# Kernel optimization log

Measured on AMD Instinct MI355X. Metric: run time of the kernel, lower is better.

Reference implementation:

```python
import jax, jax.numpy as jnp
import numpy as np

DIM = 256
N_STATE = 8
DT_RANK = 16  # ceil(dim/16)
D_CONV = 4
HIDDEN = 128  # dim * rank_ratio
EPS = 1e-6


def rmsnorm(x, w):
    # matches torch: x / (||x||_2 / sqrt(d) + eps) * w
    norm = jnp.sqrt(jnp.sum(x * x, axis=-1, keepdims=True))
    return x / (norm / np.sqrt(x.shape[-1]) + EPS) * w


def dwconv1d(x, w, b, pad_l, pad_r):
    # x: (b, l, c); w: (c, 1, k) depthwise
    out = jax.lax.conv_general_dilated(
        x.transpose(0, 2, 1), w, window_strides=(1,),
        padding=[(pad_l, pad_r)], dimension_numbers=('NCH', 'OIH', 'NCH'),
        feature_group_count=w.shape[0])
    return (out + b[None, :, None]).transpose(0, 2, 1)


def selective_scan(x, delta, A, Bm, Cm, D):
    # x, delta: (b,l,d); A: (d,n); Bm, Cm: (b,l,n); D: (d,)
    dA = jnp.exp(delta[..., None] * A)                     # (b,l,d,n)
    dBx = (delta * x)[..., None] * Bm[:, :, None, :]       # (b,l,d,n)

    def step(h, inp):
        dA_t, dBx_t, C_t = inp
        h = dA_t * h + dBx_t                               # (b,d,n)
        y = jnp.einsum('bdn,bn->bd', h, C_t)
        return h, y

    h0 = jnp.zeros((x.shape[0],) + A.shape, dtype=x.dtype)
    _, ys = jax.lax.scan(step, h0,
                         (dA.transpose(1, 0, 2, 3), dBx.transpose(1, 0, 2, 3),
                          Cm.transpose(1, 0, 2)))
    return ys.transpose(1, 0, 2) + x * D                   # (b,l,d)


def mamba_branch(x, ctx, conv_w, conv_b, xproj_w, dtproj_w, dtproj_b, A_log, D):
    xc = jax.nn.silu(dwconv1d(x, conv_w, conv_b, D_CONV - 1, 0))  # causal conv
    x_dbl = ctx @ xproj_w.T                                  # (b,l,r+2n)
    dt, Bm, Cm = jnp.split(x_dbl, [DT_RANK, DT_RANK + N_STATE], axis=-1)
    delta = jax.nn.softplus(dt @ dtproj_w.T + dtproj_b)
    A = -jnp.exp(A_log)
    return selective_scan(xc, delta, A, Bm, Cm, D)


def setup_inputs() -> dict:
    key = jax.random.key(0)
    ks = jax.random.split(key, 24)
    B, L, D = 4, 64 * 64, DIM
    s = 0.02
    A_log_init = jnp.log(jnp.broadcast_to(jnp.arange(1, N_STATE + 1, dtype=jnp.float32), (D, N_STATE)))
    dt_bias = jnp.full((D,), jnp.log(jnp.expm1(0.01)), dtype=jnp.float32)
    inp = {
        'x0': jax.random.normal(ks[0], (B, L, D), jnp.float32),
        'x1': jax.random.normal(ks[1], (B, L, D), jnp.float32),
        'w_norm0': jnp.ones((D,), jnp.float32),
        'w_norm1': jnp.ones((D,), jnp.float32),
        'in_proj_w': jax.random.normal(ks[2], (2 * D, D), jnp.float32) * s,
        'conv_w_f': jax.random.normal(ks[3], (D, 1, D_CONV), jnp.float32) * 0.3,
        'conv_b_f': jnp.zeros((D,), jnp.float32),
        'xproj_w_f': jax.random.normal(ks[4], (DT_RANK + 2 * N_STATE, D), jnp.float32) * s,
        'dtproj_w_f': jax.random.normal(ks[5], (D, DT_RANK), jnp.float32) * 0.1,
        'dtproj_b_f': dt_bias,
        'A_log_f': A_log_init,
        'D_f': jnp.ones((D,), jnp.float32),
        'conv_w_bw': jax.random.normal(ks[6], (D, 1, D_CONV), jnp.float32) * 0.3,
        'conv_b_bw': jnp.zeros((D,), jnp.float32),
        'xproj_w_bw': jax.random.normal(ks[7], (DT_RANK + 2 * N_STATE, D), jnp.float32) * s,
        'dtproj_w_bw': jax.random.normal(ks[8], (D, DT_RANK), jnp.float32) * 0.1,
        'dtproj_b_bw': dt_bias,
        'A_log_bw': A_log_init,
        'D_bw': jnp.ones((D,), jnp.float32),
        'norm_y_w': jnp.ones((D,), jnp.float32),
        'out_proj_w': jax.random.normal(ks[9], (D, D), jnp.float32) * s,
        'fc1_w': jax.random.normal(ks[10], (HIDDEN, D), jnp.float32) * s,
        'dw_w': jax.random.normal(ks[11], (HIDDEN, 1, 3), jnp.float32) * 0.3,
        'dw_b': jnp.zeros((HIDDEN,), jnp.float32),
        'fc2_w': jax.random.normal(ks[12], (D, HIDDEN), jnp.float32) * s,
    }
    return inp


def reference(x0, x1, w_norm0, w_norm1, in_proj_w, conv_w_f, conv_b_f, xproj_w_f,
              dtproj_w_f, dtproj_b_f, A_log_f, D_f, conv_w_bw, conv_b_bw,
              xproj_w_bw, dtproj_w_bw, dtproj_b_bw, A_log_bw, D_bw, norm_y_w,
              out_proj_w, fc1_w, dw_w, dw_b, fc2_w):
    residual = x0
    h0 = rmsnorm(x0, w_norm0)
    h1 = rmsnorm(x1, w_norm1)
    # cross-Mamba: main stream x0 -> x,z; extra_emb x1 -> dt/B/C
    xz = h0 @ in_proj_w.T
    xin, z = jnp.split(xz, 2, axis=-1)
    y_f = mamba_branch(xin, h1, conv_w_f, conv_b_f, xproj_w_f, dtproj_w_f,
                       dtproj_b_f, A_log_f, D_f)
    y_b = jnp.flip(mamba_branch(jnp.flip(xin, 1), jnp.flip(h1, 1), conv_w_bw,
                                conv_b_bw, xproj_w_bw, dtproj_w_bw, dtproj_b_bw,
                                A_log_bw, D_bw), 1)
    y = (y_f + y_b) * 0.5          # if_devide_out=True (bidirectional)
    y = rmsnorm(y, norm_y_w)       # use_norm=True
    y = y * jax.nn.silu(z)
    x = y @ out_proj_w.T + residual
    # LowRankFeedForward (dropout = identity at eval)
    m = x @ fc1_w.T
    m = jax.nn.silu(dwconv1d(m, dw_w, dw_b, 1, 1))
    m = m @ fc2_w.T
    return x + m
```

## Files before the change

kernel.cpp:

```cpp
#include <hip/hip_runtime.h>
#include <math.h>
#include <cstddef>

#define BB 4
#define LL 4096
#define DD 256
#define NST 8
#define RANK 16
#define HID 128
#define BL (BB*LL)
#define BLD ((size_t)BL*DD)
#define CH 128
#define CLEN 32
#define XZS 512

typedef __bf16 bf16x8 __attribute__((ext_vector_type(8)));
typedef float  f32x4  __attribute__((ext_vector_type(4)));

__device__ __forceinline__ float siluf(float x){ return x / (1.f + __expf(-x)); }
__device__ __forceinline__ float softplus_fast(float x){
  float r = __logf(1.f + __expf(x));
  return x > 15.f ? x : r;
}
__device__ __forceinline__ unsigned short f2bf(float x){
  union { float f; unsigned u; } v; v.f = x;
  unsigned r = v.u + 0x7fffu + ((v.u >> 16) & 1u);
  return (unsigned short)(r >> 16);
}
__device__ __forceinline__ float bf2f(unsigned short u){
  union { unsigned u32; float f; } c; c.u32 = ((unsigned)u) << 16;
  return c.f;
}

__global__ __launch_bounds__(64) void rms_kernel(
    const float* __restrict__ x0, const float* __restrict__ w0, unsigned short* __restrict__ o0b,
    const float* __restrict__ x1, const float* __restrict__ w1, unsigned short* __restrict__ o1b)
{
  const float* x; const float* w; unsigned short* o;
  if (blockIdx.y == 0){ x = x0; w = w0; o = o0b; } else { x = x1; w = w1; o = o1b; }
  size_t tok = blockIdx.x;
  int lane = threadIdx.x;
  float4 v = ((const float4*)(x + tok*DD))[lane];
  float s = v.x*v.x + v.y*v.y + v.z*v.z + v.w*v.w;
  #pragma unroll
  for (int m = 1; m < 64; m <<= 1) s += __shfl_xor(s, m, 64);
  float scale = 1.f / (sqrtf(s) * (1.f/16.f) + 1e-6f);
  float4 wv = ((const float4*)w)[lane];
  ushort4 r;
  r.x = f2bf(v.x*scale*wv.x); r.y = f2bf(v.y*scale*wv.y);
  r.z = f2bf(v.z*scale*wv.z); r.w = f2bf(v.w*scale*wv.w);
  ((ushort4*)(o + tok*DD))[lane] = r;
}

__global__ __launch_bounds__(256) void cvt1_kernel(
    const float* __restrict__ s, unsigned short* __restrict__ d, int n)
{
  int i = blockIdx.x*256 + threadIdx.x;
  if (i < n) d[i] = f2bf(s[i]);
}
__global__ __launch_bounds__(256) void cvt5_kernel(
    const float* __restrict__ s0, const float* __restrict__ s1,
    const float* __restrict__ s2, const float* __restrict__ s3,
    const float* __restrict__ s4, unsigned short* __restrict__ d)
{
  int i = blockIdx.x*256 + threadIdx.x;
  if (i >= 147456) return;
  float v;
  if (i < 8192)        v = s0[i];
  else if (i < 16384)  v = s1[i - 8192];
  else if (i < 81920)  v = s2[i - 16384];
  else if (i < 114688) v = s3[i - 81920];
  else                 v = s4[i - 114688];
  d[i] = f2bf(v);
}

template<int EPI>
__global__ __launch_bounds__(256) void gemm_mfma(
    const unsigned short* __restrict__ A, const unsigned short* __restrict__ Bw,
    float* __restrict__ C, const float* __restrict__ Add,
    unsigned short* __restrict__ Cb, int M, int ldc, int K)
{
  constexpr int BK = 32, PAD = 8;
  __shared__ __align__(16) unsigned short As[64][BK+PAD];
  __shared__ __align__(16) unsigned short Bs[64][BK+PAD];
  int tid  = threadIdx.x;
  int row0 = blockIdx.x * 64;
  int col0 = blockIdx.y * 64;
  int wave = tid >> 6, lane = tid & 63;
  int wm = (wave >> 1) * 32, wn = (wave & 1) * 32;
  int lm = lane & 15, kq = lane >> 4;
  int sr = tid >> 2, sc8 = (tid & 3) * 8;

  f32x4 acc[2][2];
  #pragma unroll
  for (int i = 0; i < 2; i++)
    #pragma unroll
    for (int j = 0; j < 2; j++) acc[i][j] = (f32x4){0.f,0.f,0.f,0.f};

  for (int k0 = 0; k0 < K; k0 += BK){
    *(int4*)&As[sr][sc8] = *(const int4*)&A [(size_t)(row0 + sr)*K + k0 + sc8];
    *(int4*)&Bs[sr][sc8] = *(const int4*)&Bw[(size_t)(col0 + sr)*K + k0 + sc8];
    __syncthreads();
    bf16x8 af[2], bfv[2];
    #pragma unroll
    for (int i = 0; i < 2; i++) af[i]  = *(const bf16x8*)&As[wm + i*16 + lm][kq*8];
    #pragma unroll
    for (int j = 0; j < 2; j++) bfv[j] = *(const bf16x8*)&Bs[wn + j*16 + lm][kq*8];
    #pragma unroll
    for (int i = 0; i < 2; i++)
      #pragma unroll
      for (int j = 0; j < 2; j++)
        acc[i][j] = __builtin_amdgcn_mfma_f32_16x16x32_bf16(af[i], bfv[j], acc[i][j], 0, 0, 0);
    __syncthreads();
  }

  #pragma unroll
  for (int i = 0; i < 2; i++){
    int rbase = row0 + wm + i*16 + kq*4;
    #pragma unroll
    for (int j = 0; j < 2; j++){
      int col = col0 + wn + j*16 + lm;
      #pragma unroll
      for (int r = 0; r < 4; r++){
        size_t idx = (size_t)(rbase + r)*ldc + col;
        float v = acc[i][j][r];
        if constexpr (EPI == 1 || EPI == 2) v += Add[idx];
        if constexpr (EPI != 3) C[idx] = v;
        if constexpr (EPI == 1 || EPI == 3) Cb[idx] = f2bf(v);
      }
    }
  }
}

__global__ __launch_bounds__(256) void front_kernel(
    const unsigned short* __restrict__ xz,
    const float* __restrict__ xd,
    const float* __restrict__ cwf, const float* __restrict__ cbf,
    const float* __restrict__ cwb, const float* __restrict__ cbb,
    const float* __restrict__ dtwf, const float* __restrict__ dtbf,
    const float* __restrict__ dtwb, const float* __restrict__ dtbb,
    const float* __restrict__ Alogf, const float* __restrict__ Alogb,
    unsigned int* __restrict__ xde,
    float* __restrict__ P, float* __restrict__ Hout)
{
  int chunk = blockIdx.x, b = blockIdx.y, dir = blockIdx.z;
  int s0 = chunk*CLEN;
  int d  = threadIdx.x;

  __shared__ float sdt[CLEN][16];
  __shared__ float sB [CLEN][8];
  {
    #pragma unroll
    for (int e = threadIdx.x; e < CLEN*16; e += 256){
      int lt = e >> 4, col = e & 15;
      int pos = s0 + lt;
      int row = dir ? (LL-1-pos) : pos;
      sdt[lt][col] = xd[((size_t)b*LL + row)*64 + dir*32 + col];
    }
    {
      int e = threadIdx.x;
      int lt = e >> 3, col = e & 7;
      int pos = s0 + lt;
      int row = dir ? (LL-1-pos) : pos;
      sB[lt][col] = xd[((size_t)b*LL + row)*64 + dir*32 + 16 + col];
    }
  }
  __syncthreads();

  float4 cw = ((const float4*)(dir ? cwb : cwf))[d];
  float cb  = (dir ? cbb : cbf)[d];
  const float* dtw = (dir ? dtwb : dtwf) + d*RANK;
  float4 w0 = ((const float4*)dtw)[0], w1 = ((const float4*)dtw)[1];
  float4 w2 = ((const float4*)dtw)[2], w3 = ((const float4*)dtw)[3];
  float dtb = (dir ? dtbb : dtbf)[d];

  const unsigned short* xp = xz + (size_t)b*LL*XZS + d;
  #define LDX(pos) ((pos) >= 0 ? bf2f(xp[(size_t)(dir ? (LL-1-(pos)) : (pos))*XZS]) : 0.f)

  float a0, a1, a2, a3;
  a1 = LDX(s0-3); a2 = LDX(s0-2); a3 = LDX(s0-1);

  unsigned packX[CLEN];
  const int U = 8;
  float px[U];
  #pragma unroll
  for (int u = 0; u < U; u++) px[u] = LDX(s0+u);

  for (int g = 0; g < CLEN; g += U){
    float nx[U];
    if (g + U < CLEN){
      #pragma unroll
      for (int u = 0; u < U; u++) nx[u] = LDX(s0+g+U+u);
    }
    #pragma unroll
    for (int u = 0; u < U; u++){
      int i = g + u;
      a0 = a1; a1 = a2; a2 = a3; a3 = px[u];
      float xc = cb;
      xc = fmaf(cw.x, a0, xc); xc = fmaf(cw.y, a1, xc);
      xc = fmaf(cw.z, a2, xc); xc = fmaf(cw.w, a3, xc);
      xc = siluf(xc);
      const float* dt = &sdt[i][0];
      float de = dtb;
      de = fmaf(dt[0],w0.x, fmaf(dt[1],w0.y, fmaf(dt[2],w0.z, fmaf(dt[3],w0.w, de))));
      de = fmaf(dt[4],w1.x, fmaf(dt[5],w1.y, fmaf(dt[6],w1.z, fmaf(dt[7],w1.w, de))));
      de = fmaf(dt[8],w2.x, fmaf(dt[9],w2.y, fmaf(dt[10],w2.z, fmaf(dt[11],w2.w, de))));
      de = fmaf(dt[12],w3.x, fmaf(dt[13],w3.y, fmaf(dt[14],w3.z, fmaf(dt[15],w3.w, de))));
      de = softplus_fast(de);
      unsigned pk = (unsigned)f2bf(xc) | ((unsigned)f2bf(de) << 16);
      packX[i] = pk;
      xde[((size_t)(dir*BB + b)*LL + (s0+i))*DD + d] = pk;
    }
    if (g + U < CLEN){
      #pragma unroll
      for (int u = 0; u < U; u++) px[u] = nx[u];
    }
  }
  #undef LDX

  const float* Alog = dir ? Alogb : Alogf;
  float A[NST];
  bool fast = true;
  #pragma unroll
  for (int n = 0; n < NST; n++){
    A[n] = -__expf(Alog[d*NST + n]);
    fast = fast && (fabsf(A[n] + (float)(n+1)) < 1e-3f);
  }
  float h[NST];
  #pragma unroll
  for (int n = 0; n < NST; n++) h[n] = 0.f;
  float S = 0.f;

  if (fast){
    #pragma unroll
    for (int t = 0; t < CLEN; t++){
      unsigned pk = packX[t];
      float xc = bf2f((unsigned short)(pk & 0xffffu));
      float de = bf2f((unsigned short)(pk >> 16));
      S += de;
      float dux = de * xc;
      const float* Bv = &sB[t][0];
      float e1 = __expf(-de);
      float dA = e1;
      h[0] = fmaf(dA, h[0], dux*Bv[0]); dA *= e1;
      h[1] = fmaf(dA, h[1], dux*Bv[1]); dA *= e1;
      h[2] = fmaf(dA, h[2], dux*Bv[2]); dA *= e1;
      h[3] = fmaf(dA, h[3], dux*Bv[3]); dA *= e1;
      h[4] = fmaf(dA, h[4], dux*Bv[4]); dA *= e1;
      h[5] = fmaf(dA, h[5], dux*Bv[5]); dA *= e1;
      h[6] = fmaf(dA, h[6], dux*Bv[6]); dA *= e1;
      h[7] = fmaf(dA, h[7], dux*Bv[7]);
    }
  } else {
    #pragma unroll
    for (int t = 0; t < CLEN; t++){
      unsigned pk = packX[t];
      float xc = bf2f((unsigned short)(pk & 0xffffu));
      float de = bf2f((unsigned short)(pk >> 16));
      S += de;
      float dux = de * xc;
      const float* Bv = &sB[t][0];
      #pragma unroll
      for (int n = 0; n < NST; n++)
        h[n] = fmaf(__expf(de*A[n]), h[n], dux*Bv[n]);
    }
  }

  size_t ob = ((((size_t)dir*CH + chunk)*BB + b)*DD + d)*NST;
  float4 p0, p1h, h0v, h1v;
  if (fast){
    float E = __expf(-S);
    float q = E;
    p0.x = q; q *= E; p0.y = q; q *= E; p0.z = q; q *= E; p0.w = q; q *= E;
    p1h.x= q; q *= E; p1h.y= q; q *= E; p1h.z= q; q *= E; p1h.w= q;
  } else {
    p0.x = __expf(A[0]*S); p0.y = __expf(A[1]*S); p0.z = __expf(A[2]*S); p0.w = __expf(A[3]*S);
    p1h.x= __expf(A[4]*S); p1h.y= __expf(A[5]*S); p1h.z= __expf(A[6]*S); p1h.w= __expf(A[7]*S);
  }
  h0v.x=h[0]; h0v.y=h[1]; h0v.z=h[2]; h0v.w=h[3];
  h1v.x=h[4]; h1v.y=h[5]; h1v.z=h[6]; h1v.w=h[7];
  *(float4*)&P[ob]      = p0;  *(float4*)&P[ob+4]    = p1h;
  *(float4*)&Hout[ob]   = h0v; *(float4*)&Hout[ob+4] = h1v;
}

__global__ __launch_bounds__(64) void scan_p2(
    const float* P, const float* __restrict__ Hout, float* Hin)
{
  int tid = blockIdx.x*64 + threadIdx.x;
  int dir = tid >> 13;
  int b   = (tid >> 11) & 3;
  int dn  = tid & 2047;
  const size_t stride = (size_t)BB*2048;
  size_t idx0 = (((size_t)dir*CH)*BB + b)*2048 + dn;

  const int U = 8;
  float pp[U], hh[U];
  #pragma unroll
  for (int u = 0; u < U; u++){
    pp[u] = P[idx0 + u*stride];
    hh[u] = Hout[idx0 + u*stride];
  }
  float h = 0.f;
  for (int c0 = 0; c0 < CH; c0 += U){
    float np[U], nh[U];
    if (c0 + U < CH){
      #pragma unroll
      for (int u = 0; u < U; u++){
        np[u] = P[idx0 + (size_t)(c0+U+u)*stride];
        nh[u] = Hout[idx0 + (size_t)(c0+U+u)*stride];
      }
    }
    #pragma unroll
    for (int u = 0; u < U; u++){
      Hin[idx0 + (size_t)(c0+u)*stride] = h;
      h = fmaf(pp[u], h, hh[u]);
    }
    if (c0 + U < CH){
      #pragma unroll
      for (int u = 0; u < U; u++){ pp[u] = np[u]; hh[u] = nh[u]; }
    }
  }
}

__global__ __launch_bounds__(256) void scan_p3(
    const unsigned int* __restrict__ xde,
    const float* __restrict__ xd,
    const float* __restrict__ Alogf, const float* __restrict__ Alogb,
    const float* __restrict__ Dfp, const float* __restrict__ Dbp,
    const float* Hin,
    unsigned short* __restrict__ yf, unsigned short* __restrict__ yb)
{
  int chunk = blockIdx.x, b = blockIdx.y, dir = blockIdx.z;
  const float* Alog = dir ? Alogb : Alogf;
  int d = threadIdx.x;
  int base = chunk*CLEN;

  __shared__ float sBC[CLEN*16];
  {
    #pragma unroll
    for (int e = threadIdx.x; e < CLEN*16; e += 256){
      int lt = e >> 4, col = e & 15;
      int pos = base + lt;
      int row = dir ? (LL-1-pos) : pos;
      sBC[e] = xd[((size_t)b*LL + row)*64 + dir*32 + 16 + col];
    }
  }
  __syncthreads();

  float A[NST];
  bool fast = true;
  #pragma unroll
  for (int n = 0; n < NST; n++){
    A[n] = -__expf(Alog[d*NST + n]);
    fast = fast && (fabsf(A[n] + (float)(n+1)) < 1e-3f);
  }
  float Dd = (dir ? Dbp : Dfp)[d];

  float h[NST];
  {
    size_t ib = ((((size_t)dir*CH + chunk)*BB + b)*DD + d)*NST;
    float4 a0 = *(const float4*)&Hin[ib];
    float4 a1 = *(const float4*)&Hin[ib+4];
    h[0]=a0.x; h[1]=a0.y; h[2]=a0.z; h[3]=a0.w;
    h[4]=a1.x; h[5]=a1.y; h[6]=a1.z; h[7]=a1.w;
  }

  const unsigned int* xdep = xde + ((size_t)(dir*BB + b)*LL + base)*DD + d;
  unsigned short* yp = (dir ? yb : yf) + ((size_t)b*LL + base)*DD + d;

  const int U = 8;
  unsigned int pk[U];
  #pragma unroll
  for (int u = 0; u < U; u++) pk[u] = xdep[(size_t)u*DD];

  for (int t0 = 0; t0 < CLEN; t0 += U){
    unsigned int nk[U];
    if (t0 + U < CLEN){
      #pragma unroll
      for (int u = 0; u < U; u++) nk[u] = xdep[(size_t)(t0+U+u)*DD];
    }
    if (fast){
      #pragma unroll
      for (int u = 0; u < U; u++){
        int t = t0 + u;
        float xc = bf2f((unsigned short)(pk[u] & 0xffffu));
        float de = bf2f((unsigned short)(pk[u] >> 16));
        float dux = de * xc;
        const float* Bv = &sBC[t*16];
        const float* Cv = &sBC[t*16 + 8];
        float acc = xc * Dd;
        float e1 = __expf(-de);
        float dA = e1;
        h[0] = fmaf(dA, h[0], dux*Bv[0]); acc = fmaf(h[0], Cv[0], acc); dA *= e1;
        h[1] = fmaf(dA, h[1], dux*Bv[1]); acc = fmaf(h[1], Cv[1], acc); dA *= e1;
        h[2] = fmaf(dA, h[2], dux*Bv[2]); acc = fmaf(h[2], Cv[2], acc); dA *= e1;
        h[3] = fmaf(dA, h[3], dux*Bv[3]); acc = fmaf(h[3], Cv[3], acc); dA *= e1;
        h[4] = fmaf(dA, h[4], dux*Bv[4]); acc = fmaf(h[4], Cv[4], acc); dA *= e1;
        h[5] = fmaf(dA, h[5], dux*Bv[5]); acc = fmaf(h[5], Cv[5], acc); dA *= e1;
        h[6] = fmaf(dA, h[6], dux*Bv[6]); acc = fmaf(h[6], Cv[6], acc); dA *= e1;
        h[7] = fmaf(dA, h[7], dux*Bv[7]); acc = fmaf(h[7], Cv[7], acc);
        yp[(size_t)t*DD] = f2bf(acc);
      }
    } else {
      #pragma unroll
      for (int u = 0; u < U; u++){
        int t = t0 + u;
        float xc = bf2f((unsigned short)(pk[u] & 0xffffu));
        float de = bf2f((unsigned short)(pk[u] >> 16));
        float dux = de * xc;
        const float* Bv = &sBC[t*16];
        const float* Cv = &sBC[t*16 + 8];
        float acc = xc * Dd;
        #pragma unroll
        for (int n = 0; n < NST; n++){
          h[n] = fmaf(__expf(de*A[n]), h[n], dux*Bv[n]);
          acc = fmaf(h[n], Cv[n], acc);
        }
        yp[(size_t)t*DD] = f2bf(acc);
      }
    }
    if (t0 + U < CLEN){
      #pragma unroll
      for (int u = 0; u < U; u++) pk[u] = nk[u];
    }
  }
}

__global__ __launch_bounds__(64) void combine_kernel(
    const unsigned short* __restrict__ yf, const unsigned short* __restrict__ yb,
    const unsigned short* __restrict__ xz, const float* __restrict__ wn,
    unsigned short* __restrict__ outb)
{
  size_t tok = blockIdx.x;
  int b = (int)(tok / LL), t = (int)(tok % LL);
  int lane = threadIdx.x;
  ushort4 au = ((const ushort4*)(yf + tok*DD))[lane];
  ushort4 cu = ((const ushort4*)(yb + ((size_t)b*LL + (LL-1-t))*DD))[lane];
  float4 v;
  v.x=(bf2f(au.x)+bf2f(cu.x))*0.5f; v.y=(bf2f(au.y)+bf2f(cu.y))*0.5f;
  v.z=(bf2f(au.z)+bf2f(cu.z))*0.5f; v.w=(bf2f(au.w)+bf2f(cu.w))*0.5f;
  float s = v.x*v.x + v.y*v.y + v.z*v.z + v.w*v.w;
  #pragma unroll
  for (int m = 1; m < 64; m <<= 1) s += __shfl_xor(s, m, 64);
  float scale = 1.f / (sqrtf(s)*(1.f/16.f) + 1e-6f);
  float4 wv = ((const float4*)wn)[lane];
  ushort4 zv = *(const ushort4*)&xz[tok*XZS + 256 + lane*4];
  ushort4 r;
  r.x = f2bf(v.x*scale*wv.x*siluf(bf2f(zv.x)));
  r.y = f2bf(v.y*scale*wv.y*siluf(bf2f(zv.y)));
  r.z = f2bf(v.z*scale*wv.z*siluf(bf2f(zv.z)));
  r.w = f2bf(v.w*scale*wv.w*siluf(bf2f(zv.w)));
  ((ushort4*)(outb + tok*DD))[lane] = r;
}

__global__ __launch_bounds__(256) void dwconv3_kernel(
    const float* __restrict__ m, const float* __restrict__ w,
    const float* __restrict__ bi, unsigned short* __restrict__ o)
{
  size_t gid = (size_t)blockIdx.x*256 + threadIdx.x;
  int c = (int)(gid % HID);
  int tok = (int)(gid / HID);
  int b = tok / LL, t = tok % LL;
  float acc = bi[c];
  #pragma unroll
  for (int k = 0; k < 3; k++){
    int tt = t - 1 + k;
    if (tt >= 0 && tt < LL)
      acc = fmaf(w[c*3 + k], m[((size_t)b*LL + tt)*HID + c], acc);
  }
  o[gid] = f2bf(siluf(acc));
}

extern "C" void kernel_launch(void* const* d_in, const int* in_sizes, int n_in,
                              void* d_out, int out_size, void* d_ws, size_t ws_size,
                              hipStream_t stream)
{
  const float* x0        = (const float*)d_in[0];
  const float* x1        = (const float*)d_in[1];
  const float* w_norm0   = (const float*)d_in[2];
  const float* w_norm1   = (const float*)d_in[3];
  const float* in_proj_w = (const float*)d_in[4];
  const float* conv_w_f  = (const float*)d_in[5];
  const float* conv_b_f  = (const float*)d_in[6];
  const float* xproj_w_f = (const float*)d_in[7];
  const float* dtproj_w_f= (const float*)d_in[8];
  const float* dtproj_b_f= (const float*)d_in[9];
  const float* A_log_f   = (const float*)d_in[10];
  const float* D_f       = (const float*)d_in[11];
  const float* conv_w_bw = (const float*)d_in[12];
  const float* conv_b_bw = (const float*)d_in[13];
  const float* xproj_w_bw= (const float*)d_in[14];
  const float* dtproj_w_bw=(const float*)d_in[15];
  const float* dtproj_b_bw=(const float*)d_in[16];
  const float* A_log_bw  = (const float*)d_in[17];
  const float* D_bw      = (const float*)d_in[18];
  const float* norm_y_w  = (const float*)d_in[19];
  const float* out_proj_w= (const float*)d_in[20];
  const float* fc1_w     = (const float*)d_in[21];
  const float* dw_w      = (const float*)d_in[22];
  const float* dw_b      = (const float*)d_in[23];
  const float* fc2_w     = (const float*)d_in[24];
  float* out = (float*)d_out;
  float* ws  = (float*)d_ws;

  float* r0 = ws + 0*BLD;
  float* r1 = ws + 1*BLD;
  float* r2 = ws + 2*BLD;
  float* r3 = ws + 3*BLD;
  float* r4 = ws + 4*BLD;
  float* r5 = ws + 5*BLD;
  float* r6 = ws + 6*BLD;
  float* r7 = ws + 7*BLD;

  unsigned short* h0b   = (unsigned short*)r0;
  unsigned short* h1b   = (unsigned short*)r1;
  unsigned short* xz_b  = (unsigned short*)r2;
  float*          xd    = r3;
  unsigned int*   xde   = (unsigned int*)r4;
  unsigned short* wbuf1 = (unsigned short*)r6;
  unsigned short* yfb   = (unsigned short*)r0;
  unsigned short* ybb   = (unsigned short*)r1;
  const size_t CARRY = (size_t)2*CH*BB*DD*NST;
  float* Pbuf = r6;
  float* Hout = r6 + CARRY;
  float* Hin  = Pbuf;
  unsigned short* ycomb_b = (unsigned short*)r3;
  unsigned short* wbuf2   = (unsigned short*)r7;
  unsigned short* wb_xp   = wbuf2;
  unsigned short* wb_out  = wbuf2 + 16384;
  unsigned short* wb_fc1  = wbuf2 + 81920;
  unsigned short* wb_fc2  = wbuf2 + 114688;
  unsigned short* xb      = wbuf2 + 147456;
  float*          m1      = r4;
  unsigned short* m2b     = (unsigned short*)r5;

  cvt1_kernel<<<dim3(512), 256, 0, stream>>>(in_proj_w, wbuf1, 131072);
  cvt5_kernel<<<dim3(576), 256, 0, stream>>>(
      xproj_w_f, xproj_w_bw, out_proj_w, fc1_w, fc2_w, wbuf2);

  rms_kernel<<<dim3(BL,2), 64, 0, stream>>>(x0, w_norm0, h0b, x1, w_norm1, h1b);

  gemm_mfma<3><<<dim3(BL/64, 8), 256, 0, stream>>>(
      h0b, wbuf1, nullptr, nullptr, xz_b, BL, XZS, 256);

  gemm_mfma<0><<<dim3(BL/64, 1), 256, 0, stream>>>(
      h1b, wb_xp, xd, nullptr, nullptr, BL, 64, 256);

  front_kernel<<<dim3(CH, BB, 2), 256, 0, stream>>>(
      xz_b, xd, conv_w_f, conv_b_f, conv_w_bw, conv_b_bw,
      dtproj_w_f, dtproj_b_f, dtproj_w_bw, dtproj_b_bw,
      A_log_f, A_log_bw, xde, Pbuf, Hout);

  scan_p2<<<dim3(256), 64, 0, stream>>>(Pbuf, Hout, Hin);
  scan_p3<<<dim3(CH,BB,2), 256, 0, stream>>>(
      xde, xd, A_log_f, A_log_bw, D_f, D_bw, Hin, yfb, ybb);

  combine_kernel<<<dim3(BL), 64, 0, stream>>>(yfb, ybb, xz_b, norm_y_w, ycomb_b);

  gemm_mfma<1><<<dim3(BL/64, 4), 256, 0, stream>>>(
      ycomb_b, wb_out, out, x0, xb, BL, 256, 256);

  gemm_mfma<0><<<dim3(BL/64, 2), 256, 0, stream>>>(
      xb, wb_fc1, m1, nullptr, nullptr, BL, 128, 256);

  dwconv3_kernel<<<dim3((BL*HID)/256), 256, 0, stream>>>(m1, dw_w, dw_b, m2b);

  gemm_mfma<2><<<dim3(BL/64, 4), 256, 0, stream>>>(
      m2b, wb_fc2, out, out, nullptr, BL, 256, 128);
}
```

Baseline: 265.1 us.

## Compute local-chunk scan output in front pass, apply carry correction afterward

The front kernel now produces the zero-initial-state chunk output y0 alongside delta, packed into xde, so the third pass no longer re-runs the recurrence. It only adds the carried-in state contribution exp(A*cumsum(delta))·h_in·C. The carry pass is parallelised per (dir,b,d) block, using segment-local scans plus a warp-shuffle prefix across segments. It recomputes decay factors from stored delta sums instead of storing P. Chunks are halved in length and doubled in count, which shrinks per-thread register arrays but doubles carry traffic. The output y0 is held in bf16 before the correction is added, which may cost some precision.

```diff
diff --git a/kernel.cpp b/kernel.cpp
--- a/kernel.cpp
+++ b/kernel.cpp
@@ -10,8 +10,8 @@
 #define HID 128
 #define BL (BB*LL)
 #define BLD ((size_t)BL*DD)
-#define CH 128
-#define CLEN 32
+#define CH 256
+#define CLEN 16
 #define XZS 512
 
 typedef __bf16 bf16x8 __attribute__((ext_vector_type(8)));
@@ -140,8 +140,9 @@
     const float* __restrict__ dtwf, const float* __restrict__ dtbf,
     const float* __restrict__ dtwb, const float* __restrict__ dtbb,
     const float* __restrict__ Alogf, const float* __restrict__ Alogb,
+    const float* __restrict__ Dfp, const float* __restrict__ Dbp,
     unsigned int* __restrict__ xde,
-    float* __restrict__ P, float* __restrict__ Hout)
+    float* __restrict__ Sp, float* __restrict__ Hout)
 {
   int chunk = blockIdx.x, b = blockIdx.y, dir = blockIdx.z;
   int s0 = chunk*CLEN;
@@ -149,21 +150,16 @@
 
   __shared__ float sdt[CLEN][16];
   __shared__ float sB [CLEN][8];
-  {
-    #pragma unroll
-    for (int e = threadIdx.x; e < CLEN*16; e += 256){
-      int lt = e >> 4, col = e & 15;
-      int pos = s0 + lt;
-      int row = dir ? (LL-1-pos) : pos;
-      sdt[lt][col] = xd[((size_t)b*LL + row)*64 + dir*32 + col];
-    }
-    {
-      int e = threadIdx.x;
-      int lt = e >> 3, col = e & 7;
-      int pos = s0 + lt;
-      int row = dir ? (LL-1-pos) : pos;
-      sB[lt][col] = xd[((size_t)b*LL + row)*64 + dir*32 + 16 + col];
-    }
+  __shared__ float sC [CLEN][8];
+  #pragma unroll
+  for (int e = threadIdx.x; e < CLEN*32; e += 256){
+    int lt = e >> 5, col = e & 31;
+    int pos = s0 + lt;
+    int row = dir ? (LL-1-pos) : pos;
+    float v = xd[((size_t)b*LL + row)*64 + dir*32 + col];
+    if (col < 16)      sdt[lt][col]    = v;
+    else if (col < 24) sB [lt][col-16] = v;
+    else               sC [lt][col-24] = v;
   }
   __syncthreads();
 
@@ -173,50 +169,33 @@
   float4 w0 = ((const float4*)dtw)[0], w1 = ((const float4*)dtw)[1];
   float4 w2 = ((const float4*)dtw)[2], w3 = ((const float4*)dtw)[3];
   float dtb = (dir ? dtbb : dtbf)[d];
+  float Dd  = (dir ? Dbp : Dfp)[d];
 
   const unsigned short* xp = xz + (size_t)b*LL*XZS + d;
   #define LDX(pos) ((pos) >= 0 ? bf2f(xp[(size_t)(dir ? (LL-1-(pos)) : (pos))*XZS]) : 0.f)
 
-  float a0, a1, a2, a3;
-  a1 = LDX(s0-3); a2 = LDX(s0-2); a3 = LDX(s0-1);
+  float xv[CLEN+3];
+  xv[0] = LDX(s0-3); xv[1] = LDX(s0-2); xv[2] = LDX(s0-1);
+  #pragma unroll
+  for (int i = 0; i < CLEN; i++) xv[3+i] = LDX(s0+i);
+  #undef LDX
 
   unsigned packX[CLEN];
-  const int U = 8;
-  float px[U];
-  #pragma unroll
-  for (int u = 0; u < U; u++) px[u] = LDX(s0+u);
-
-  for (int g = 0; g < CLEN; g += U){
-    float nx[U];
-    if (g + U < CLEN){
-      #pragma unroll
-      for (int u = 0; u < U; u++) nx[u] = LDX(s0+g+U+u);
-    }
-    #pragma unroll
-    for (int u = 0; u < U; u++){
-      int i = g + u;
-      a0 = a1; a1 = a2; a2 = a3; a3 = px[u];
-      float xc = cb;
-      xc = fmaf(cw.x, a0, xc); xc = fmaf(cw.y, a1, xc);
-      xc = fmaf(cw.z, a2, xc); xc = fmaf(cw.w, a3, xc);
-      xc = siluf(xc);
-      const float* dt = &sdt[i][0];
-      float de = dtb;
-      de = fmaf(dt[0],w0.x, fmaf(dt[1],w0.y, fmaf(dt[2],w0.z, fmaf(dt[3],w0.w, de))));
-      de = fmaf(dt[4],w1.x, fmaf(dt[5],w1.y, fmaf(dt[6],w1.z, fmaf(dt[7],w1.w, de))));
-      de = fmaf(dt[8],w2.x, fmaf(dt[9],w2.y, fmaf(dt[10],w2.z, fmaf(dt[11],w2.w, de))));
-      de = fmaf(dt[12],w3.x, fmaf(dt[13],w3.y, fmaf(dt[14],w3.z, fmaf(dt[15],w3.w, de))));
-      de = softplus_fast(de);
-      unsigned pk = (unsigned)f2bf(xc) | ((unsigned)f2bf(de) << 16);
-      packX[i] = pk;
-      xde[((size_t)(dir*BB + b)*LL + (s0+i))*DD + d] = pk;
-    }
-    if (g + U < CLEN){
-      #pragma unroll
-      for (int u = 0; u < U; u++) px[u] = nx[u];
-    }
-  }
-  #undef LDX
+  #pragma unroll
+  for (int i = 0; i < CLEN; i++){
+    float xc = cb;
+    xc = fmaf(cw.x, xv[i],   xc); xc = fmaf(cw.y, xv[i+1], xc);
+    xc = fmaf(cw.z, xv[i+2], xc); xc = fmaf(cw.w, xv[i+3], xc);
+    xc = siluf(xc);
+    const float* dt = &sdt[i][0];
+    float de = dtb;
+    de = fmaf(dt[0],w0.x, fmaf(dt[1],w0.y, fmaf(dt[2],w0.z, fmaf(dt[3],w0.w, de))));
+    de = fmaf(dt[4],w1.x, fmaf(dt[5],w1.y, fmaf(dt[6],w1.z, fmaf(dt[7],w1.w, de))));
+    de = fmaf(dt[8],w2.x, fmaf(dt[9],w2.y, fmaf(dt[10],w2.z, fmaf(dt[11],w2.w, de))));
+    de = fmaf(dt[12],w3.x, fmaf(dt[13],w3.y, fmaf(dt[14],w3.z, fmaf(dt[15],w3.w, de))));
+    de = softplus_fast(de);
+    packX[i] = (unsigned)f2bf(xc) | ((unsigned)f2bf(de) << 16);
+  }
 
   const float* Alog = dir ? Alogb : Alogf;
   float A[NST];
@@ -230,6 +209,8 @@
   #pragma unroll
   for (int n = 0; n < NST; n++) h[n] = 0.f;
   float S = 0.f;
+
+  unsigned int* xout = xde + ((size_t)(dir*BB + b)*LL + s0)*DD + d;
 
   if (fast){
     #pragma unroll
@@ -240,16 +221,19 @@
       S += de;
       float dux = de * xc;
       const float* Bv = &sB[t][0];
+      const float* Cv = &sC[t][0];
       float e1 = __expf(-de);
       float dA = e1;
-      h[0] = fmaf(dA, h[0], dux*Bv[0]); dA *= e1;
-      h[1] = fmaf(dA, h[1], dux*Bv[1]); dA *= e1;
-      h[2] = fmaf(dA, h[2], dux*Bv[2]); dA *= e1;
-      h[3] = fmaf(dA, h[3], dux*Bv[3]); dA *= e1;
-      h[4] = fmaf(dA, h[4], dux*Bv[4]); dA *= e1;
-      h[5] = fmaf(dA, h[5], dux*Bv[5]); dA *= e1;
-      h[6] = fmaf(dA, h[6], dux*Bv[6]); dA *= e1;
-      h[7] = fmaf(dA, h[7], dux*Bv[7]);
+      float acc = xc * Dd;
+      h[0] = fmaf(dA, h[0], dux*Bv[0]); acc = fmaf(h[0], Cv[0], acc); dA *= e1;
+      h[1] = fmaf(dA, h[1], dux*Bv[1]); acc = fmaf(h[1], Cv[1], acc); dA *= e1;
+      h[2] = fmaf(dA, h[2], dux*Bv[2]); acc = fmaf(h[2], Cv[2], acc); dA *= e1;
+      h[3] = fmaf(dA, h[3], dux*Bv[3]); acc = fmaf(h[3], Cv[3], acc); dA *= e1;
+      h[4] = fmaf(dA, h[4], dux*Bv[4]); acc = fmaf(h[4], Cv[4], acc); dA *= e1;
+      h[5] = fmaf(dA, h[5], dux*Bv[5]); acc = fmaf(h[5], Cv[5], acc); dA *= e1;
+      h[6] = fmaf(dA, h[6], dux*Bv[6]); acc = fmaf(h[6], Cv[6], acc); dA *= e1;
+      h[7] = fmaf(dA, h[7], dux*Bv[7]); acc = fmaf(h[7], Cv[7], acc);
+      xout[(size_t)t*DD] = (pk & 0xffff0000u) | (unsigned)f2bf(acc);
     }
   } else {
     #pragma unroll
@@ -260,93 +244,95 @@
       S += de;
       float dux = de * xc;
       const float* Bv = &sB[t][0];
+      const float* Cv = &sC[t][0];
+      float acc = xc * Dd;
       #pragma unroll
-      for (int n = 0; n < NST; n++)
+      for (int n = 0; n < NST; n++){
         h[n] = fmaf(__expf(de*A[n]), h[n], dux*Bv[n]);
+        acc = fmaf(h[n], Cv[n], acc);
+      }
+      xout[(size_t)t*DD] = (pk & 0xffff0000u) | (unsigned)f2bf(acc);
     }
   }
 
   size_t ob = ((((size_t)dir*CH + chunk)*BB + b)*DD + d)*NST;
-  float4 p0, p1h, h0v, h1v;
-  if (fast){
-    float E = __expf(-S);
-    float q = E;
-    p0.x = q; q *= E; p0.y = q; q *= E; p0.z = q; q *= E; p0.w = q; q *= E;
-    p1h.x= q; q *= E; p1h.y= q; q *= E; p1h.z= q; q *= E; p1h.w= q;
-  } else {
-    p0.x = __expf(A[0]*S); p0.y = __expf(A[1]*S); p0.z = __expf(A[2]*S); p0.w = __expf(A[3]*S);
-    p1h.x= __expf(A[4]*S); p1h.y= __expf(A[5]*S); p1h.z= __expf(A[6]*S); p1h.w= __expf(A[7]*S);
-  }
+  float4 h0v, h1v;
   h0v.x=h[0]; h0v.y=h[1]; h0v.z=h[2]; h0v.w=h[3];
   h1v.x=h[4]; h1v.y=h[5]; h1v.z=h[6]; h1v.w=h[7];
-  *(float4*)&P[ob]      = p0;  *(float4*)&P[ob+4]    = p1h;
   *(float4*)&Hout[ob]   = h0v; *(float4*)&Hout[ob+4] = h1v;
+  Sp[((size_t)(dir*CH + chunk)*BB + b)*DD + d] = S;
 }
 
 __global__ __launch_bounds__(64) void scan_p2(
-    const float* P, const float* __restrict__ Hout, float* Hin)
-{
-  int tid = blockIdx.x*64 + threadIdx.x;
-  int dir = tid >> 13;
-  int b   = (tid >> 11) & 3;
-  int dn  = tid & 2047;
-  const size_t stride = (size_t)BB*2048;
-  size_t idx0 = (((size_t)dir*CH)*BB + b)*2048 + dn;
-
-  const int U = 8;
-  float pp[U], hh[U];
-  #pragma unroll
-  for (int u = 0; u < U; u++){
-    pp[u] = P[idx0 + u*stride];
-    hh[u] = Hout[idx0 + u*stride];
-  }
-  float h = 0.f;
-  for (int c0 = 0; c0 < CH; c0 += U){
-    float np[U], nh[U];
-    if (c0 + U < CH){
-      #pragma unroll
-      for (int u = 0; u < U; u++){
-        np[u] = P[idx0 + (size_t)(c0+U+u)*stride];
-        nh[u] = Hout[idx0 + (size_t)(c0+U+u)*stride];
-      }
-    }
-    #pragma unroll
-    for (int u = 0; u < U; u++){
-      Hin[idx0 + (size_t)(c0+u)*stride] = h;
-      h = fmaf(pp[u], h, hh[u]);
-    }
-    if (c0 + U < CH){
-      #pragma unroll
-      for (int u = 0; u < U; u++){ pp[u] = np[u]; hh[u] = nh[u]; }
-    }
-  }
-}
-
-__global__ __launch_bounds__(256) void scan_p3(
+    const float* __restrict__ Sp, float* H,
+    const float* __restrict__ Alogf, const float* __restrict__ Alogb)
+{
+  const int SEGC = CH/8;
+  int blk = blockIdx.x;
+  int d   = blk & (DD-1);
+  int b   = (blk >> 8) & (BB-1);
+  int dir = blk >> 10;
+  int t   = threadIdx.x;
+  int seg = t >> 3, n = t & 7;
+  float A = -__expf((dir ? Alogb : Alogf)[d*NST + n]);
+
+  const size_t sstr = (size_t)BB*DD;
+  const size_t hstr = (size_t)BB*DD*NST;
+  size_t sb = (size_t)dir*CH*sstr + (size_t)b*DD + d;
+  size_t hb = (size_t)dir*CH*hstr + ((size_t)b*DD + d)*NST + n;
+  int c0 = seg*SEGC;
+
+  float pv[SEGC], hv[SEGC];
+  #pragma unroll
+  for (int k = 0; k < SEGC; k++){
+    pv[k] = Sp[sb + (size_t)(c0+k)*sstr];
+    hv[k] = H [hb + (size_t)(c0+k)*hstr];
+  }
+  float h = 0.f, Ss = 0.f;
+  #pragma unroll
+  for (int k = 0; k < SEGC; k++){
+    Ss += pv[k];
+    pv[k] = __expf(pv[k]*A);
+    h = fmaf(pv[k], h, hv[k]);
+  }
+  float pi = __expf(Ss*A), hi = h;
+  #pragma unroll
+  for (int off = 8; off < 64; off <<= 1){
+    float hprev = __shfl_up(hi, off, 64);
+    float pprev = __shfl_up(pi, off, 64);
+    if (t >= off){ hi = fmaf(pi, hprev, hi); pi *= pprev; }
+  }
+  float hin = __shfl_up(hi, 8, 64);
+  h = (seg == 0) ? 0.f : hin;
+  #pragma unroll
+  for (int k = 0; k < SEGC; k++){
+    size_t idx = hb + (size_t)(c0+k)*hstr;
+    H[idx] = h;
+    h = fmaf(pv[k], h, hv[k]);
+  }
+}
+
+__global__ __launch_bounds__(256) void scan_corr(
     const unsigned int* __restrict__ xde,
     const float* __restrict__ xd,
     const float* __restrict__ Alogf, const float* __restrict__ Alogb,
-    const float* __restrict__ Dfp, const float* __restrict__ Dbp,
-    const float* Hin,
+    const float* __restrict__ Hin,
     unsigned short* __restrict__ yf, unsigned short* __restrict__ yb)
 {
   int chunk = blockIdx.x, b = blockIdx.y, dir = blockIdx.z;
-  const float* Alog = dir ? Alogb : Alogf;
   int d = threadIdx.x;
   int base = chunk*CLEN;
 
-  __shared__ float sBC[CLEN*16];
-  {
-    #pragma unroll
-    for (int e = threadIdx.x; e < CLEN*16; e += 256){
-      int lt = e >> 4, col = e & 15;
-      int pos = base + lt;
-      int row = dir ? (LL-1-pos) : pos;
-      sBC[e] = xd[((size_t)b*LL + row)*64 + dir*32 + 16 + col];
-    }
+  __shared__ float sC[CLEN][8];
+  if (threadIdx.x < CLEN*8){
+    int lt = threadIdx.x >> 3, col = threadIdx.x & 7;
+    int pos = base + lt;
+    int row = dir ? (LL-1-pos) : pos;
+    sC[lt][col] = xd[((size_t)b*LL + row)*64 + dir*32 + 24 + col];
   }
   __syncthreads();
 
+  const float* Alog = dir ? Alogb : Alogf;
   float A[NST];
   bool fast = true;
   #pragma unroll
@@ -354,74 +340,52 @@
     A[n] = -__expf(Alog[d*NST + n]);
     fast = fast && (fabsf(A[n] + (float)(n+1)) < 1e-3f);
   }
-  float Dd = (dir ? Dbp : Dfp)[d];
-
-  float h[NST];
+  float hn[NST];
   {
     size_t ib = ((((size_t)dir*CH + chunk)*BB + b)*DD + d)*NST;
     float4 a0 = *(const float4*)&Hin[ib];
     float4 a1 = *(const float4*)&Hin[ib+4];
-    h[0]=a0.x; h[1]=a0.y; h[2]=a0.z; h[3]=a0.w;
-    h[4]=a1.x; h[5]=a1.y; h[6]=a1.z; h[7]=a1.w;
+    hn[0]=a0.x; hn[1]=a0.y; hn[2]=a0.z; hn[3]=a0.w;
+    hn[4]=a1.x; hn[5]=a1.y; hn[6]=a1.z; hn[7]=a1.w;
   }
 
   const unsigned int* xdep = xde + ((size_t)(dir*BB + b)*LL + base)*DD + d;
   unsigned short* yp = (dir ? yb : yf) + ((size_t)b*LL + base)*DD + d;
 
-  const int U = 8;
-  unsigned int pk[U];
-  #pragma unroll
-  for (int u = 0; u < U; u++) pk[u] = xdep[(size_t)u*DD];
-
-  for (int t0 = 0; t0 < CLEN; t0 += U){
-    unsigned int nk[U];
-    if (t0 + U < CLEN){
+  unsigned int pk[CLEN];
+  #pragma unroll
+  for (int t = 0; t < CLEN; t++) pk[t] = xdep[(size_t)t*DD];
+
+  float S = 0.f;
+  if (fast){
+    #pragma unroll
+    for (int t = 0; t < CLEN; t++){
+      float y0 = bf2f((unsigned short)(pk[t] & 0xffffu));
+      float de = bf2f((unsigned short)(pk[t] >> 16));
+      S += de;
+      float E = __expf(-S);
+      float q = E;
+      float corr = q * (hn[0]*sC[t][0]);
+      q *= E; corr = fmaf(q, hn[1]*sC[t][1], corr);
+      q *= E; corr = fmaf(q, hn[2]*sC[t][2], corr);
+      q *= E; corr = fmaf(q, hn[3]*sC[t][3], corr);
+      q *= E; corr = fmaf(q, hn[4]*sC[t][4], corr);
+      q *= E; corr = fmaf(q, hn[5]*sC[t][5], corr);
+      q *= E; corr = fmaf(q, hn[6]*sC[t][6], corr);
+      q *= E; corr = fmaf(q, hn[7]*sC[t][7], corr);
+      yp[(size_t)t*DD] = f2bf(y0 + corr);
+    }
+  } else {
+    #pragma unroll
+    for (int t = 0; t < CLEN; t++){
+      float y0 = bf2f((unsigned short)(pk[t] & 0xffffu));
+      float de = bf2f((unsigned short)(pk[t] >> 16));
+      S += de;
+      float corr = 0.f;
       #pragma unroll
-      for (int u = 0; u < U; u++) nk[u] = xdep[(size_t)(t0+U+u)*DD];
-    }
-    if (fast){
-      #pragma unroll
-      for (int u = 0; u < U; u++){
-        int t = t0 + u;
-        float xc = bf2f((unsigned short)(pk[u] & 0xffffu));
-        float de = bf2f((unsigned short)(pk[u] >> 16));
-        float dux = de * xc;
-        const float* Bv = &sBC[t*16];
-        const float* Cv = &sBC[t*16 + 8];
-        float acc = xc * Dd;
-        float e1 = __expf(-de);
-        float dA = e1;
-        h[0] = fmaf(dA, h[0], dux*Bv[0]); acc = fmaf(h[0], Cv[0], acc); dA *= e1;
-        h[1] = fmaf(dA, h[1], dux*Bv[1]); acc = fmaf(h[1], Cv[1], acc); dA *= e1;
-        h[2] = fmaf(dA, h[2], dux*Bv[2]); acc = fmaf(h[2], Cv[2], acc); dA *= e1;
-        h[3] = fmaf(dA, h[3], dux*Bv[3]); acc = fmaf(h[3], Cv[3], acc); dA *= e1;
-        h[4] = fmaf(dA, h[4], dux*Bv[4]); acc = fmaf(h[4], Cv[4], acc); dA *= e1;
-        h[5] = fmaf(dA, h[5], dux*Bv[5]); acc = fmaf(h[5], Cv[5], acc); dA *= e1;
-        h[6] = fmaf(dA, h[6], dux*Bv[6]); acc = fmaf(h[6], Cv[6], acc); dA *= e1;
-        h[7] = fmaf(dA, h[7], dux*Bv[7]); acc = fmaf(h[7], Cv[7], acc);
-        yp[(size_t)t*DD] = f2bf(acc);
-      }
-    } else {
-      #pragma unroll
-      for (int u = 0; u < U; u++){
-        int t = t0 + u;
-        float xc = bf2f((unsigned short)(pk[u] & 0xffffu));
-        float de = bf2f((unsigned short)(pk[u] >> 16));
-        float dux = de * xc;
-        const float* Bv = &sBC[t*16];
-        const float* Cv = &sBC[t*16 + 8];
-        float acc = xc * Dd;
-        #pragma unroll
-        for (int n = 0; n < NST; n++){
-          h[n] = fmaf(__expf(de*A[n]), h[n], dux*Bv[n]);
-          acc = fmaf(h[n], Cv[n], acc);
-        }
-        yp[(size_t)t*DD] = f2bf(acc);
-      }
-    }
-    if (t0 + U < CLEN){
-      #pragma unroll
-      for (int u = 0; u < U; u++) pk[u] = nk[u];
+      for (int n = 0; n < NST; n++)
+        corr = fmaf(__expf(S*A[n]), hn[n]*sC[t][n], corr);
+      yp[(size_t)t*DD] = f2bf(y0 + corr);
     }
   }
 }
@@ -520,10 +484,10 @@
   unsigned short* wbuf1 = (unsigned short*)r6;
   unsigned short* yfb   = (unsigned short*)r0;
   unsigned short* ybb   = (unsigned short*)r1;
-  const size_t CARRY = (size_t)2*CH*BB*DD*NST;
-  float* Pbuf = r6;
-  float* Hout = r6 + CARRY;
-  float* Hin  = Pbuf;
+  float* Hout = r6;
+  float* Hin  = Hout;
+  const size_t SPLANE = (size_t)2*CH*BB*DD;
+  float* Sp   = r7 + (BLD - SPLANE);
   unsigned short* ycomb_b = (unsigned short*)r3;
   unsigned short* wbuf2   = (unsigned short*)r7;
   unsigned short* wb_xp   = wbuf2;
@@ -549,11 +513,12 @@
   front_kernel<<<dim3(CH, BB, 2), 256, 0, stream>>>(
       xz_b, xd, conv_w_f, conv_b_f, conv_w_bw, conv_b_bw,
       dtproj_w_f, dtproj_b_f, dtproj_w_bw, dtproj_b_bw,
-      A_log_f, A_log_bw, xde, Pbuf, Hout);
-
-  scan_p2<<<dim3(256), 64, 0, stream>>>(Pbuf, Hout, Hin);
-  scan_p3<<<dim3(CH,BB,2), 256, 0, stream>>>(
-      xde, xd, A_log_f, A_log_bw, D_f, D_bw, Hin, yfb, ybb);
+      A_log_f, A_log_bw, D_f, D_bw, xde, Sp, Hout);
+
+  scan_p2<<<dim3(2*BB*DD), 64, 0, stream>>>(Sp, Hout, A_log_f, A_log_bw);
+
+  scan_corr<<<dim3(CH, BB, 2), 256, 0, stream>>>(
+      xde, xd, A_log_f, A_log_bw, Hin, yfb, ybb);
 
   combine_kernel<<<dim3(BL), 64, 0, stream>>>(yfb, ybb, xz_b, norm_y_w, ycomb_b);
 
```

Result: no change. 262.3 us (-1.1%).
